# Kernel tuning notes

Hardware: AMD Instinct MI355X
Metric: run time of the kernel (lower is better)

Reference implementation:

```python
import jax, jax.numpy as jnp
import numpy as np

B, S, N_USERS, N_ITEMS, E = 32, 512, 10000, 10000, 128


def setup_inputs() -> dict:
    key = jax.random.key(0)
    ks = jax.random.split(key, 8)
    users = jax.random.randint(ks[0], (B, S), 0, N_USERS, dtype=jnp.int32)
    items = jax.random.randint(ks[1], (B, S), 0, N_ITEMS, dtype=jnp.int32)
    user_mem0 = jax.random.normal(ks[2], (B, N_USERS, E), dtype=jnp.float32)
    item_mem0 = jax.random.normal(ks[3], (B, N_ITEMS, E), dtype=jnp.float32)
    # GRUCell(2E, E): w_ih (3E, 2E), w_hh (3E, E)
    w_ih = jax.random.normal(ks[4], (3 * E, 2 * E), dtype=jnp.float32) * 0.05
    w_hh = jax.random.normal(ks[5], (3 * E, E), dtype=jnp.float32) * 0.05
    b_ih = jax.random.normal(ks[6], (3 * E,), dtype=jnp.float32) * 0.05
    b_hh = jax.random.normal(ks[7], (3 * E,), dtype=jnp.float32) * 0.05
    return {"users": users, "items": items, "user_mem0": user_mem0,
            "item_mem0": item_mem0, "w_ih": w_ih, "w_hh": w_hh,
            "b_ih": b_ih, "b_hh": b_hh}


def _gru_cell(x, h, w_ih, w_hh, b_ih, b_hh):
    # torch.nn.GRUCell semantics
    gi = x @ w_ih.T + b_ih  # (B, 3E)
    gh = h @ w_hh.T + b_hh  # (B, 3E)
    i_r, i_z, i_n = jnp.split(gi, 3, axis=-1)
    h_r, h_z, h_n = jnp.split(gh, 3, axis=-1)
    r = jax.nn.sigmoid(i_r + h_r)
    z = jax.nn.sigmoid(i_z + h_z)
    n = jnp.tanh(i_n + r * h_n)
    return (1.0 - z) * n + z * h


def reference(users, items, user_mem0, item_mem0, w_ih, w_hh, b_ih, b_hh):
    batch = jnp.arange(users.shape[0])

    def step(carry, uv):
        um, im = carry
        u, it = uv  # (B,), (B,)
        ue = um[batch, u]   # gather (B, E)
        ie = im[batch, it]  # gather (B, E)
        xu = jnp.concatenate([ue, ie], axis=-1)
        xi = jnp.concatenate([ie, ue], axis=-1)
        nu = _gru_cell(xu, ue, w_ih, w_hh, b_ih, b_hh)
        ni = _gru_cell(xi, ie, w_ih, w_hh, b_ih, b_hh)
        um = um.at[batch, u].set(nu)   # scatter write
        im = im.at[batch, it].set(ni)  # scatter write
        return (um, im), (nu, ni)

    (_, _), (u_out, i_out) = jax.lax.scan(
        step, (user_mem0, item_mem0), (users.T, items.T))
    # (S, B, E) -> (B, S, E)
    return jnp.transpose(u_out, (1, 0, 2)), jnp.transpose(i_out, (1, 0, 2))
```

## Files before the change

### kernel.cpp

```cpp
#include <hip/hip_runtime.h>

#define NB 32
#define NS 512
#define NE 128
#define NU 10000

#define WS_PREVU 0
#define WS_PREVI 16384
#define WS_RCNT  32768
#define WS_LCNT  32864
#define WS_GL    32896
#define WS_LATE  82048
#define WS_WBF   98432

typedef __attribute__((ext_vector_type(8))) short bf16x8;
typedef __attribute__((ext_vector_type(4))) float f32x4;

__device__ __forceinline__ unsigned short f2bf(float f) {
    unsigned int u = __float_as_uint(f);
    u += 0x7fff + ((u >> 16) & 1);
    return (unsigned short)(u >> 16);
}

#define BARRIER() do { \
    asm volatile("s_waitcnt lgkmcnt(0)" ::: "memory"); \
    __builtin_amdgcn_s_barrier(); \
    __builtin_amdgcn_sched_barrier(0); \
} while (0)

__global__ __launch_bounds__(512) void prep_kernel(
    const int* __restrict__ users, const int* __restrict__ items,
    const float* __restrict__ w_ih, const float* __restrict__ w_hh, int* ws)
{
    const int blk = blockIdx.x, tid = threadIdx.x;
    if (blk >= 32) {
        const int base = (blk - 32) * 4096 + tid * 8;
        const int r = base >> 7, k = base & 127;
        const float* src;
        if (r < 384)      src = w_ih + (size_t)r * 256 + k;
        else if (r < 768) src = w_ih + (size_t)(r - 384) * 256 + 128 + k;
        else              src = w_hh + (size_t)(r - 768) * 128 + k;
        unsigned short* wbf = (unsigned short*)(ws + WS_WBF);
#pragma unroll
        for (int j = 0; j < 8; ++j) wbf[base + j] = f2bf(src[j]);
        return;
    }
    const int b = blk;
    __shared__ int s_u[NS], s_i[NS];
    __shared__ unsigned char s_r[NS];
    __shared__ int cnt[3], s_chg;
    s_u[tid] = users[b * NS + tid];
    s_i[tid] = items[b * NS + tid];
    if (tid < 3) cnt[tid] = 0;
    __syncthreads();
    const int mu = s_u[tid], mi = s_i[tid];
    int pu = -1, pi = -1;
    for (int u = tid - 1; u >= 0 && pu < 0; u -= 8) {
        int vals[8];
#pragma unroll
        for (int j = 0; j < 8; ++j) {
            const int uu = u - j;
            vals[j] = (uu >= 0) ? s_u[uu] : -1;
        }
#pragma unroll
        for (int j = 0; j < 8; ++j)
            if (pu < 0 && vals[j] == mu) pu = u - j;
    }
    for (int u = tid - 1; u >= 0 && pi < 0; u -= 8) {
        int vals[8];
#pragma unroll
        for (int j = 0; j < 8; ++j) {
            const int uu = u - j;
            vals[j] = (uu >= 0) ? s_i[uu] : -1;
        }
#pragma unroll
        for (int j = 0; j < 8; ++j)
            if (pi < 0 && vals[j] == mi) pi = u - j;
    }
    ws[WS_PREVU + (b << 9) + tid] = pu;
    ws[WS_PREVI + (b << 9) + tid] = pi;
    s_r[tid] = (pu < 0 && pi < 0) ? 0 : 255;
    __syncthreads();
    for (int pass = 0; pass < 16; ++pass) {
        if (tid == 0) s_chg = 0;
        __syncthreads();
        if (s_r[tid] == 255) {
            const int ru = pu < 0 ? -1 : (int)s_r[pu];
            const int ri = pi < 0 ? -1 : (int)s_r[pi];
            if (ru != 255 && ri != 255) {
                int rr = 1 + (ru > ri ? ru : ri);
                if (rr > 3) rr = 3;
                s_r[tid] = (unsigned char)rr;
                s_chg = 1;
            }
        }
        __syncthreads();
        if (!s_chg) break;
    }
    const int r = s_r[tid];
    if (r < 3) {
        const int slot = atomicAdd(&cnt[r], 1);
        ws[WS_GL + (r * 32 + b) * 512 + slot] = tid;
    }
    __syncthreads();
    if (tid < 3) ws[WS_RCNT + tid * 32 + b] = cnt[tid];
    if (tid == 0) {
        int n = 0;
        for (int t = 0; t < NS; ++t)
            if (s_r[t] >= 3) { ws[WS_LATE + (b << 9) + n] = t; ++n; }
        ws[WS_LCNT + b] = n;
    }
}

__global__ __launch_bounds__(512, 1) void round_gemm(
    const int* __restrict__ users, const int* __restrict__ items,
    const float* __restrict__ umem0, const float* __restrict__ imem0,
    const float* __restrict__ b_ih, const float* __restrict__ b_hh,
    const int* __restrict__ ws, float* uout, float* iout, int r)
{
    const int b = blockIdx.x & 31, sblk = blockIdx.x >> 5;
    const int cnt = ws[WS_RCNT + r * 32 + b];
    const int nch = (cnt + 7) >> 3;
    if (sblk >= nch) return;
    const int tid = threadIdx.x;
    const int lane = tid & 63, wave = tid >> 6;
    const int col = lane & 15, kgrp = lane >> 4;

    __shared__ __align__(16) float yl[16 * 1156];
    __shared__ __align__(16) float xf[16 * 132];
    __shared__ __align__(16) unsigned short xb[16 * 136];
    __shared__ float b6[768];
    __shared__ unsigned long long srcs[8][16];
    __shared__ unsigned long long hdst[8][16];

    for (int i = tid; i < 768; i += 512)
        b6[i] = i < 384 ? b_ih[i] : b_hh[i - 384];

    const unsigned short* wbf = (const unsigned short*)(ws + WS_WBF);
    bf16x8 wfrag[9][4];
#pragma unroll
    for (int m9 = 0; m9 < 9; ++m9) {
        const int row = wave * 144 + m9 * 16 + col;
#pragma unroll
        for (int kt = 0; kt < 4; ++kt)
            wfrag[m9][kt] = *(const bf16x8*)&wbf[row * 128 + kt * 32 + kgrp * 8];
    }

    const int* glist = ws + WS_GL + (r * 32 + b) * 512;
    const int* prevU = ws + WS_PREVU + (b << 9);
    const int* prevI = ws + WS_PREVI + (b << 9);

    if (tid < 128) {
        const int k = tid >> 4, idx = tid & 15;
        const int lc = sblk + k * 8;
        unsigned long long sp = 0, hd = 0;
        if (lc < nch) {
            const int j = lc * 8 + (idx >> 1);
            if (j < cnt) {
                const int t = glist[j];
                const int node = (b << 9) + t;
                const int cell = idx & 1;
                const int p = cell ? prevI[t] : prevU[t];
                const float* s;
                if (p < 0) {
                    const int ix = cell ? items[node] : users[node];
                    s = (cell ? imem0 : umem0) + ((size_t)b * NU + ix) * NE;
                } else {
                    s = (cell ? iout : uout) + ((size_t)((b << 9) + p)) * NE;
                }
                sp = (unsigned long long)s;
                hd = (unsigned long long)((cell ? iout : uout) + (size_t)node * NE);
            }
        }
        srcs[k][idx] = sp; hdst[k][idx] = hd;
    }
    BARRIER();

    const int gc = tid >> 5, ge4 = (tid & 31) * 4;
    float4 v[8];
#pragma unroll
    for (int k = 0; k < 8; ++k) {
        const float* s = (const float*)srcs[k][gc];
        v[k] = (float4){0.f, 0.f, 0.f, 0.f};
        if (s) v[k] = *(const float4*)(s + ge4);
    }

#pragma unroll
    for (int k = 0; k < 8; ++k) {
        const int lc = sblk + k * 8;
        if (lc >= nch) break;
        if (srcs[k][gc]) {
            *(float4*)&xf[gc * 132 + ge4] = v[k];
            ushort4 w4;
            w4.x = f2bf(v[k].x); w4.y = f2bf(v[k].y);
            w4.z = f2bf(v[k].z); w4.w = f2bf(v[k].w);
            *(ushort4*)&xb[gc * 136 + ge4] = w4;
        }
        BARRIER();
        {
            bf16x8 bfrag[4];
#pragma unroll
            for (int kt = 0; kt < 4; ++kt)
                bfrag[kt] = *(const bf16x8*)&xb[col * 136 + kt * 32 + kgrp * 8];
            f32x4 acc[9];
#pragma unroll
            for (int m9 = 0; m9 < 9; ++m9) acc[m9] = (f32x4){0.f, 0.f, 0.f, 0.f};
#pragma unroll
            for (int kt = 0; kt < 4; ++kt)
#pragma unroll
                for (int m9 = 0; m9 < 9; ++m9)
                    acc[m9] = __builtin_amdgcn_mfma_f32_16x16x32_bf16(
                        wfrag[m9][kt], bfrag[kt], acc[m9], 0, 0, 0);
#pragma unroll
            for (int m9 = 0; m9 < 9; ++m9)
                *(f32x4*)&yl[col * 1156 + wave * 144 + m9 * 16 + kgrp * 4] = acc[m9];
        }
        BARRIER();
#pragma unroll
        for (int it = 0; it < 4; ++it) {
            const int idx = tid + it * 512;
            const int c = idx >> 7, e = idx & 127;
            float* hb = (float*)hdst[k][c];
            if (hb) {
                const float* ys = &yl[c * 1156];
                const float* yo = &yl[(c ^ 1) * 1156];
                const float gir = ys[e]        + yo[384 + e] + b6[e];
                const float giz = ys[128 + e]  + yo[512 + e] + b6[128 + e];
                const float gin = ys[256 + e]  + yo[640 + e] + b6[256 + e];
                const float ghr = ys[768 + e]  + b6[384 + e];
                const float ghz = ys[896 + e]  + b6[512 + e];
                const float ghn = ys[1024 + e] + b6[640 + e];
                const float rr = 1.f / (1.f + __expf(-(gir + ghr)));
                const float z  = 1.f / (1.f + __expf(-(giz + ghz)));
                const float pre = gin + rr * ghn;
                const float n = 2.f / (1.f + __expf(-2.f * pre)) - 1.f;
                hb[e] = (1.f - z) * n + z * xf[c * 132 + e];
            }
        }
        BARRIER();
    }
}

__global__ __launch_bounds__(512, 1) void cleanup_kernel(
    const int* __restrict__ users, const int* __restrict__ items,
    const float* __restrict__ umem0, const float* __restrict__ imem0,
    const float* __restrict__ b_ih, const float* __restrict__ b_hh,
    const int* __restrict__ ws, float* uout, float* iout)
{
    const int b = blockIdx.x;
    const int n = ws[WS_LCNT + b];
    if (n == 0) return;
    const int tid = threadIdx.x;
    const int lane = tid & 63, wave = tid >> 6;
    const int col = lane & 15, kgrp = lane >> 4;

    __shared__ __align__(16) float yl[2][1156];
    __shared__ __align__(16) float xf[2][132];
    __shared__ __align__(16) unsigned short xb[2][136];
    __shared__ float b6[768];
    __shared__ const float* srcs[2];

    for (int i = tid; i < 768; i += 512)
        b6[i] = i < 384 ? b_ih[i] : b_hh[i - 384];

    const unsigned short* wbf = (const unsigned short*)(ws + WS_WBF);
    bf16x8 wfrag[9][4];
#pragma unroll
    for (int m9 = 0; m9 < 9; ++m9) {
        const int row = wave * 144 + m9 * 16 + col;
#pragma unroll
        for (int kt = 0; kt < 4; ++kt)
            wfrag[m9][kt] = *(const bf16x8*)&wbf[row * 128 + kt * 32 + kgrp * 8];
    }

    const int* prevU = ws + WS_PREVU + (b << 9);
    const int* prevI = ws + WS_PREVI + (b << 9);

    for (int k = 0; k < n; ++k) {
        const int t = ws[WS_LATE + (b << 9) + k];
        const int node = (b << 9) + t;
        if (tid < 2) {
            const int cell = tid;
            const int p = cell ? prevI[t] : prevU[t];
            const float* sp;
            if (p < 0) {
                const int ix = cell ? items[node] : users[node];
                sp = (cell ? imem0 : umem0) + ((size_t)b * NU + ix) * NE;
            } else {
                sp = (cell ? iout : uout) + ((size_t)((b << 9) + p)) * NE;
            }
            srcs[cell] = sp;
        }
        __syncthreads();
        if (tid < 64) {
            const int c = tid >> 5, e4 = (tid & 31) * 4;
            const float4 vv = *(const float4*)(srcs[c] + e4);
            *(float4*)&xf[c][e4] = vv;
            ushort4 w4;
            w4.x = f2bf(vv.x); w4.y = f2bf(vv.y);
            w4.z = f2bf(vv.z); w4.w = f2bf(vv.w);
            *(ushort4*)&xb[c][e4] = w4;
        }
        __syncthreads();
        {
            const int bc = col & 1;
            bf16x8 bfrag[4];
#pragma unroll
            for (int kt = 0; kt < 4; ++kt)
                bfrag[kt] = *(const bf16x8*)&xb[bc][kt * 32 + kgrp * 8];
            f32x4 acc[9];
#pragma unroll
            for (int m9 = 0; m9 < 9; ++m9) acc[m9] = (f32x4){0.f, 0.f, 0.f, 0.f};
#pragma unroll
            for (int kt = 0; kt < 4; ++kt)
#pragma unroll
                for (int m9 = 0; m9 < 9; ++m9)
                    acc[m9] = __builtin_amdgcn_mfma_f32_16x16x32_bf16(
                        wfrag[m9][kt], bfrag[kt], acc[m9], 0, 0, 0);
            if (col < 2) {
#pragma unroll
                for (int m9 = 0; m9 < 9; ++m9)
                    *(f32x4*)&yl[col][wave * 144 + m9 * 16 + kgrp * 4] = acc[m9];
            }
        }
        __syncthreads();
        if (tid < 256) {
            const int c = tid >> 7, e = tid & 127;
            const float* ys = yl[c];
            const float* yo = yl[c ^ 1];
            const float gir = ys[e]        + yo[384 + e] + b6[e];
            const float giz = ys[128 + e]  + yo[512 + e] + b6[128 + e];
            const float gin = ys[256 + e]  + yo[640 + e] + b6[256 + e];
            const float ghr = ys[768 + e]  + b6[384 + e];
            const float ghz = ys[896 + e]  + b6[512 + e];
            const float ghn = ys[1024 + e] + b6[640 + e];
            const float rr = 1.f / (1.f + __expf(-(gir + ghr)));
            const float z  = 1.f / (1.f + __expf(-(giz + ghz)));
            const float pre = gin + rr * ghn;
            const float nn = 2.f / (1.f + __expf(-2.f * pre)) - 1.f;
            (c ? iout : uout)[(size_t)node * NE + e] =
                (1.f - z) * nn + z * xf[c][e];
        }
        __threadfence();
        __syncthreads();
    }
}

extern "C" void kernel_launch(void* const* d_in, const int* in_sizes, int n_in,
                              void* d_out, int out_size, void* d_ws, size_t ws_size,
                              hipStream_t stream) {
    const int*   users = (const int*)d_in[0];
    const int*   items = (const int*)d_in[1];
    const float* umem0 = (const float*)d_in[2];
    const float* imem0 = (const float*)d_in[3];
    const float* w_ih  = (const float*)d_in[4];
    const float* w_hh  = (const float*)d_in[5];
    const float* b_ih  = (const float*)d_in[6];
    const float* b_hh  = (const float*)d_in[7];

    float* uout = (float*)d_out;
    float* iout = uout + (size_t)NB * NS * NE;
    int* ws = (int*)d_ws;

    prep_kernel<<<68, 512, 0, stream>>>(users, items, w_ih, w_hh, ws);
    round_gemm<<<256, 512, 0, stream>>>(users, items, umem0, imem0,
                                        b_ih, b_hh, ws, uout, iout, 0);
    round_gemm<<<256, 512, 0, stream>>>(users, items, umem0, imem0,
                                        b_ih, b_hh, ws, uout, iout, 1);
    round_gemm<<<256, 512, 0, stream>>>(users, items, umem0, imem0,
                                        b_ih, b_hh, ws, uout, iout, 2);
    cleanup_kernel<<<NB, 512, 0, stream>>>(users, items, umem0, imem0,
                                           b_ih, b_hh, ws, uout, iout);
}
```

Measured before the change: 135.4 us.

## Fuse round and cleanup kernels into one persistent kernel with per-node ready flags

Replaces the three per-round GEMM launches and the serial cleanup launch with a single persistent kernel. Its 256 blocks walk a flattened work list of round chunks followed by late nodes. Dependencies between steps are enforced by per-node completion flags in workspace, using spin-waits with sleep and release via atomicExch after a threadfence. This removes launch gaps and lets the late tail run on many blocks instead of one block per batch. The cost is that each chunk is now processed alone rather than eight chunks sharing one load phase, plus spin-wait overhead and a deadlock risk if the dependency order is violated.

```diff
diff --git a/kernel.cpp b/kernel.cpp
--- a/kernel.cpp
+++ b/kernel.cpp
@@ -12,6 +12,7 @@
 #define WS_GL    32896
 #define WS_LATE  82048
 #define WS_WBF   98432
+#define WS_FLAG  172160
 
 typedef __attribute__((ext_vector_type(8))) short bf16x8;
 typedef __attribute__((ext_vector_type(4))) float f32x4;
@@ -43,6 +44,8 @@
         unsigned short* wbf = (unsigned short*)(ws + WS_WBF);
 #pragma unroll
         for (int j = 0; j < 8; ++j) wbf[base + j] = f2bf(src[j]);
+        const int fidx = (blk - 32) * 512 + tid;
+        if (fidx < 16384) ws[WS_FLAG + fidx] = 0;
         return;
     }
     const int b = blk;
@@ -112,16 +115,12 @@
     }
 }
 
-__global__ __launch_bounds__(512, 1) void round_gemm(
+__global__ __launch_bounds__(512, 1) void solve_kernel(
     const int* __restrict__ users, const int* __restrict__ items,
     const float* __restrict__ umem0, const float* __restrict__ imem0,
     const float* __restrict__ b_ih, const float* __restrict__ b_hh,
-    const int* __restrict__ ws, float* uout, float* iout, int r)
+    int* ws, float* uout, float* iout)
 {
-    const int b = blockIdx.x & 31, sblk = blockIdx.x >> 5;
-    const int cnt = ws[WS_RCNT + r * 32 + b];
-    const int nch = (cnt + 7) >> 3;
-    if (sblk >= nch) return;
     const int tid = threadIdx.x;
     const int lane = tid & 63, wave = tid >> 6;
     const int col = lane & 15, kgrp = lane >> 4;
@@ -130,11 +129,13 @@
     __shared__ __align__(16) float xf[16 * 132];
     __shared__ __align__(16) unsigned short xb[16 * 136];
     __shared__ float b6[768];
-    __shared__ unsigned long long srcs[8][16];
-    __shared__ unsigned long long hdst[8][16];
+    __shared__ int s_cnt[128];
+    __shared__ unsigned long long srcs[16];
+    __shared__ unsigned long long hdst[16];
 
     for (int i = tid; i < 768; i += 512)
         b6[i] = i < 384 ? b_ih[i] : b_hh[i - 384];
+    if (tid < 128) s_cnt[tid] = ws[WS_RCNT + tid];
 
     const unsigned short* wbf = (const unsigned short*)(ws + WS_WBF);
     bf16x8 wfrag[9][4];
@@ -145,58 +146,71 @@
         for (int kt = 0; kt < 4; ++kt)
             wfrag[m9][kt] = *(const bf16x8*)&wbf[row * 128 + kt * 32 + kgrp * 8];
     }
-
-    const int* glist = ws + WS_GL + (r * 32 + b) * 512;
-    const int* prevU = ws + WS_PREVU + (b << 9);
-    const int* prevI = ws + WS_PREVI + (b << 9);
-
-    if (tid < 128) {
-        const int k = tid >> 4, idx = tid & 15;
-        const int lc = sblk + k * 8;
-        unsigned long long sp = 0, hd = 0;
-        if (lc < nch) {
-            const int j = lc * 8 + (idx >> 1);
-            if (j < cnt) {
-                const int t = glist[j];
+    __syncthreads();
+
+    for (int v = blockIdx.x; v < 22528; v += 256) {
+        int base, n, b;
+        if (v < 6144) {
+            const int r = v >> 11, lc = v & 63;
+            b = (v >> 6) & 31;
+            const int cnt = s_cnt[r * 32 + b];
+            const int nch = (cnt + 7) >> 3;
+            if (lc >= nch) continue;
+            base = WS_GL + (r * 32 + b) * 512 + lc * 8;
+            n = cnt - lc * 8; if (n > 8) n = 8;
+        } else {
+            const int v2 = v - 6144, k = v2 & 511;
+            b = v2 >> 9;
+            if (k >= s_cnt[96 + b]) continue;
+            base = WS_LATE + (b << 9) + k;
+            n = 1;
+        }
+
+        int haspar = 0;
+        if (tid < 16) {
+            const int j = tid >> 1;
+            unsigned long long sp = 0, hd = 0;
+            if (j < n) {
+                const int t = ws[base + j];
                 const int node = (b << 9) + t;
-                const int cell = idx & 1;
-                const int p = cell ? prevI[t] : prevU[t];
+                const int cell = tid & 1;
+                const int p = ws[(cell ? WS_PREVI : WS_PREVU) + (b << 9) + t];
                 const float* s;
                 if (p < 0) {
                     const int ix = cell ? items[node] : users[node];
                     s = (cell ? imem0 : umem0) + ((size_t)b * NU + ix) * NE;
                 } else {
                     s = (cell ? iout : uout) + ((size_t)((b << 9) + p)) * NE;
+                    haspar = 1;
+                    int* fp = ws + WS_FLAG + (b << 9) + p;
+                    int spins = 0;
+                    while (atomicAdd(fp, 0) == 0) {
+                        __builtin_amdgcn_s_sleep(2);
+                        if (++spins > (1 << 24)) break;
+                    }
                 }
                 sp = (unsigned long long)s;
                 hd = (unsigned long long)((cell ? iout : uout) + (size_t)node * NE);
             }
-        }
-        srcs[k][idx] = sp; hdst[k][idx] = hd;
-    }
-    BARRIER();
-
-    const int gc = tid >> 5, ge4 = (tid & 31) * 4;
-    float4 v[8];
-#pragma unroll
-    for (int k = 0; k < 8; ++k) {
-        const float* s = (const float*)srcs[k][gc];
-        v[k] = (float4){0.f, 0.f, 0.f, 0.f};
-        if (s) v[k] = *(const float4*)(s + ge4);
-    }
-
-#pragma unroll
-    for (int k = 0; k < 8; ++k) {
-        const int lc = sblk + k * 8;
-        if (lc >= nch) break;
-        if (srcs[k][gc]) {
-            *(float4*)&xf[gc * 132 + ge4] = v[k];
-            ushort4 w4;
-            w4.x = f2bf(v[k].x); w4.y = f2bf(v[k].y);
-            w4.z = f2bf(v[k].z); w4.w = f2bf(v[k].w);
-            *(ushort4*)&xb[gc * 136 + ge4] = w4;
+            srcs[tid] = sp; hdst[tid] = hd;
+        }
+        if (__syncthreads_count(haspar))
+            __threadfence();
+
+        {
+            const int c = tid >> 5, e4 = (tid & 31) * 4;
+            const float* s = (const float*)srcs[c];
+            if (s) {
+                const float4 vv = *(const float4*)(s + e4);
+                *(float4*)&xf[c * 132 + e4] = vv;
+                ushort4 w4;
+                w4.x = f2bf(vv.x); w4.y = f2bf(vv.y);
+                w4.z = f2bf(vv.z); w4.w = f2bf(vv.w);
+                *(ushort4*)&xb[c * 136 + e4] = w4;
+            }
         }
         BARRIER();
+
         {
             bf16x8 bfrag[4];
 #pragma unroll
@@ -216,11 +230,12 @@
                 *(f32x4*)&yl[col * 1156 + wave * 144 + m9 * 16 + kgrp * 4] = acc[m9];
         }
         BARRIER();
+
 #pragma unroll
         for (int it = 0; it < 4; ++it) {
             const int idx = tid + it * 512;
             const int c = idx >> 7, e = idx & 127;
-            float* hb = (float*)hdst[k][c];
+            float* hb = (float*)hdst[c];
             if (hb) {
                 const float* ys = &yl[c * 1156];
                 const float* yo = &yl[(c ^ 1) * 1156];
@@ -233,116 +248,17 @@
                 const float rr = 1.f / (1.f + __expf(-(gir + ghr)));
                 const float z  = 1.f / (1.f + __expf(-(giz + ghz)));
                 const float pre = gin + rr * ghn;
-                const float n = 2.f / (1.f + __expf(-2.f * pre)) - 1.f;
-                hb[e] = (1.f - z) * n + z * xf[c * 132 + e];
-            }
-        }
-        BARRIER();
-    }
-}
-
-__global__ __launch_bounds__(512, 1) void cleanup_kernel(
-    const int* __restrict__ users, const int* __restrict__ items,
-    const float* __restrict__ umem0, const float* __restrict__ imem0,
-    const float* __restrict__ b_ih, const float* __restrict__ b_hh,
-    const int* __restrict__ ws, float* uout, float* iout)
-{
-    const int b = blockIdx.x;
-    const int n = ws[WS_LCNT + b];
-    if (n == 0) return;
-    const int tid = threadIdx.x;
-    const int lane = tid & 63, wave = tid >> 6;
-    const int col = lane & 15, kgrp = lane >> 4;
-
-    __shared__ __align__(16) float yl[2][1156];
-    __shared__ __align__(16) float xf[2][132];
-    __shared__ __align__(16) unsigned short xb[2][136];
-    __shared__ float b6[768];
-    __shared__ const float* srcs[2];
-
-    for (int i = tid; i < 768; i += 512)
-        b6[i] = i < 384 ? b_ih[i] : b_hh[i - 384];
-
-    const unsigned short* wbf = (const unsigned short*)(ws + WS_WBF);
-    bf16x8 wfrag[9][4];
-#pragma unroll
-    for (int m9 = 0; m9 < 9; ++m9) {
-        const int row = wave * 144 + m9 * 16 + col;
-#pragma unroll
-        for (int kt = 0; kt < 4; ++kt)
-            wfrag[m9][kt] = *(const bf16x8*)&wbf[row * 128 + kt * 32 + kgrp * 8];
-    }
-
-    const int* prevU = ws + WS_PREVU + (b << 9);
-    const int* prevI = ws + WS_PREVI + (b << 9);
-
-    for (int k = 0; k < n; ++k) {
-        const int t = ws[WS_LATE + (b << 9) + k];
-        const int node = (b << 9) + t;
-        if (tid < 2) {
-            const int cell = tid;
-            const int p = cell ? prevI[t] : prevU[t];
-            const float* sp;
-            if (p < 0) {
-                const int ix = cell ? items[node] : users[node];
-                sp = (cell ? imem0 : umem0) + ((size_t)b * NU + ix) * NE;
-            } else {
-                sp = (cell ? iout : uout) + ((size_t)((b << 9) + p)) * NE;
-            }
-            srcs[cell] = sp;
-        }
-        __syncthreads();
-        if (tid < 64) {
-            const int c = tid >> 5, e4 = (tid & 31) * 4;
-            const float4 vv = *(const float4*)(srcs[c] + e4);
-            *(float4*)&xf[c][e4] = vv;
-            ushort4 w4;
-            w4.x = f2bf(vv.x); w4.y = f2bf(vv.y);
-            w4.z = f2bf(vv.z); w4.w = f2bf(vv.w);
-            *(ushort4*)&xb[c][e4] = w4;
-        }
-        __syncthreads();
-        {
-            const int bc = col & 1;
-            bf16x8 bfrag[4];
-#pragma unroll
-            for (int kt = 0; kt < 4; ++kt)
-                bfrag[kt] = *(const bf16x8*)&xb[bc][kt * 32 + kgrp * 8];
-            f32x4 acc[9];
-#pragma unroll
-            for (int m9 = 0; m9 < 9; ++m9) acc[m9] = (f32x4){0.f, 0.f, 0.f, 0.f};
-#pragma unroll
-            for (int kt = 0; kt < 4; ++kt)
-#pragma unroll
-                for (int m9 = 0; m9 < 9; ++m9)
-                    acc[m9] = __builtin_amdgcn_mfma_f32_16x16x32_bf16(
-                        wfrag[m9][kt], bfrag[kt], acc[m9], 0, 0, 0);
-            if (col < 2) {
-#pragma unroll
-                for (int m9 = 0; m9 < 9; ++m9)
-                    *(f32x4*)&yl[col][wave * 144 + m9 * 16 + kgrp * 4] = acc[m9];
-            }
-        }
-        __syncthreads();
-        if (tid < 256) {
-            const int c = tid >> 7, e = tid & 127;
-            const float* ys = yl[c];
-            const float* yo = yl[c ^ 1];
-            const float gir = ys[e]        + yo[384 + e] + b6[e];
-            const float giz = ys[128 + e]  + yo[512 + e] + b6[128 + e];
-            const float gin = ys[256 + e]  + yo[640 + e] + b6[256 + e];
-            const float ghr = ys[768 + e]  + b6[384 + e];
-            const float ghz = ys[896 + e]  + b6[512 + e];
-            const float ghn = ys[1024 + e] + b6[640 + e];
-            const float rr = 1.f / (1.f + __expf(-(gir + ghr)));
-            const float z  = 1.f / (1.f + __expf(-(giz + ghz)));
-            const float pre = gin + rr * ghn;
-            const float nn = 2.f / (1.f + __expf(-2.f * pre)) - 1.f;
-            (c ? iout : uout)[(size_t)node * NE + e] =
-                (1.f - z) * nn + z * xf[c][e];
-        }
+                const float nn = 2.f / (1.f + __expf(-2.f * pre)) - 1.f;
+                hb[e] = (1.f - z) * nn + z * xf[c * 132 + e];
+            }
+        }
+
         __threadfence();
         __syncthreads();
+        if (tid < n) {
+            const int t = ws[base + tid];
+            atomicExch(ws + WS_FLAG + (b << 9) + t, 1);
+        }
     }
 }
 
@@ -363,12 +279,6 @@
     int* ws = (int*)d_ws;
 
     prep_kernel<<<68, 512, 0, stream>>>(users, items, w_ih, w_hh, ws);
-    round_gemm<<<256, 512, 0, stream>>>(users, items, umem0, imem0,
-                                        b_ih, b_hh, ws, uout, iout, 0);
-    round_gemm<<<256, 512, 0, stream>>>(users, items, umem0, imem0,
-                                        b_ih, b_hh, ws, uout, iout, 1);
-    round_gemm<<<256, 512, 0, stream>>>(users, items, umem0, imem0,
-                                        b_ih, b_hh, ws, uout, iout, 2);
-    cleanup_kernel<<<NB, 512, 0, stream>>>(users, items, umem0, imem0,
-                                           b_ih, b_hh, ws, uout, iout);
-}
+    solve_kernel<<<256, 512, 0, stream>>>(users, items, umem0, imem0,
+                                          b_ih, b_hh, ws, uout, iout);
+}
```

Measured after the change: 525.8 us. +288.3%, slower.

## Merge rounds 1-2 and cleanup into one per-batch finish kernel

Applied to the files above, without the earlier changes.

Keeps a wide round-0 kernel and replaces the round-1, round-2 and cleanup launches with a single per-batch kernel. That kernel walks rounds 1 and 2 in chunks of 8 steps, then the late steps one at a time. The intent is to save two kernel launches and their grid-wide drains. The cost is that rounds 1 and 2 now run on only 32 blocks instead of up to 256. The round-0 kernel also drops register prefetching of all chunks in favour of a simple per-chunk loop with plain __syncthreads.

```diff
diff --git a/kernel.cpp b/kernel.cpp
--- a/kernel.cpp
+++ b/kernel.cpp
@@ -21,12 +21,6 @@
     u += 0x7fff + ((u >> 16) & 1);
     return (unsigned short)(u >> 16);
 }
-
-#define BARRIER() do { \
-    asm volatile("s_waitcnt lgkmcnt(0)" ::: "memory"); \
-    __builtin_amdgcn_s_barrier(); \
-    __builtin_amdgcn_sched_barrier(0); \
-} while (0)
 
 __global__ __launch_bounds__(512) void prep_kernel(
     const int* __restrict__ users, const int* __restrict__ items,
@@ -112,14 +106,14 @@
     }
 }
 
-__global__ __launch_bounds__(512, 1) void round_gemm(
+__global__ __launch_bounds__(512, 1) void rg0_kernel(
     const int* __restrict__ users, const int* __restrict__ items,
     const float* __restrict__ umem0, const float* __restrict__ imem0,
     const float* __restrict__ b_ih, const float* __restrict__ b_hh,
-    const int* __restrict__ ws, float* uout, float* iout, int r)
+    const int* __restrict__ ws, float* uout, float* iout)
 {
     const int b = blockIdx.x & 31, sblk = blockIdx.x >> 5;
-    const int cnt = ws[WS_RCNT + r * 32 + b];
+    const int cnt = ws[WS_RCNT + b];
     const int nch = (cnt + 7) >> 3;
     if (sblk >= nch) return;
     const int tid = threadIdx.x;
@@ -130,8 +124,8 @@
     __shared__ __align__(16) float xf[16 * 132];
     __shared__ __align__(16) unsigned short xb[16 * 136];
     __shared__ float b6[768];
-    __shared__ unsigned long long srcs[8][16];
-    __shared__ unsigned long long hdst[8][16];
+    __shared__ unsigned long long srcs[16];
+    __shared__ unsigned long long hdst[16];
 
     for (int i = tid; i < 768; i += 512)
         b6[i] = i < 384 ? b_ih[i] : b_hh[i - 384];
@@ -146,57 +140,37 @@
             wfrag[m9][kt] = *(const bf16x8*)&wbf[row * 128 + kt * 32 + kgrp * 8];
     }
 
-    const int* glist = ws + WS_GL + (r * 32 + b) * 512;
-    const int* prevU = ws + WS_PREVU + (b << 9);
-    const int* prevI = ws + WS_PREVI + (b << 9);
-
-    if (tid < 128) {
-        const int k = tid >> 4, idx = tid & 15;
-        const int lc = sblk + k * 8;
-        unsigned long long sp = 0, hd = 0;
-        if (lc < nch) {
-            const int j = lc * 8 + (idx >> 1);
+    const int* glist = ws + WS_GL + b * 512;
+
+    for (int lc = sblk; lc < nch; lc += 8) {
+        if (tid < 16) {
+            const int j = lc * 8 + (tid >> 1);
+            unsigned long long sp = 0, hd = 0;
             if (j < cnt) {
                 const int t = glist[j];
                 const int node = (b << 9) + t;
-                const int cell = idx & 1;
-                const int p = cell ? prevI[t] : prevU[t];
-                const float* s;
-                if (p < 0) {
-                    const int ix = cell ? items[node] : users[node];
-                    s = (cell ? imem0 : umem0) + ((size_t)b * NU + ix) * NE;
-                } else {
-                    s = (cell ? iout : uout) + ((size_t)((b << 9) + p)) * NE;
-                }
-                sp = (unsigned long long)s;
+                const int cell = tid & 1;
+                const int ix = cell ? items[node] : users[node];
+                sp = (unsigned long long)((cell ? imem0 : umem0)
+                                          + ((size_t)b * NU + ix) * NE);
                 hd = (unsigned long long)((cell ? iout : uout) + (size_t)node * NE);
             }
-        }
-        srcs[k][idx] = sp; hdst[k][idx] = hd;
-    }
-    BARRIER();
-
-    const int gc = tid >> 5, ge4 = (tid & 31) * 4;
-    float4 v[8];
-#pragma unroll
-    for (int k = 0; k < 8; ++k) {
-        const float* s = (const float*)srcs[k][gc];
-        v[k] = (float4){0.f, 0.f, 0.f, 0.f};
-        if (s) v[k] = *(const float4*)(s + ge4);
-    }
-
-#pragma unroll
-    for (int k = 0; k < 8; ++k) {
-        const int lc = sblk + k * 8;
-        if (lc >= nch) break;
-        if (srcs[k][gc]) {
-            *(float4*)&xf[gc * 132 + ge4] = v[k];
-            ushort4 w4;
-            w4.x = f2bf(v[k].x); w4.y = f2bf(v[k].y);
-            w4.z = f2bf(v[k].z); w4.w = f2bf(v[k].w);
-            *(ushort4*)&xb[gc * 136 + ge4] = w4;
-        }
-        BARRIER();
+            srcs[tid] = sp; hdst[tid] = hd;
+        }
+        __syncthreads();
+        {
+            const int c = tid >> 5, e4 = (tid & 31) * 4;
+            const float* s = (const float*)srcs[c];
+            if (s) {
+                const float4 vv = *(const float4*)(s + e4);
+                *(float4*)&xf[c * 132 + e4] = vv;
+                ushort4 w4;
+                w4.x = f2bf(vv.x); w4.y = f2bf(vv.y);
+                w4.z = f2bf(vv.z); w4.w = f2bf(vv.w);
+                *(ushort4*)&xb[c * 136 + e4] = w4;
+            }
+        }
+        __syncthreads();
         {
             bf16x8 bfrag[4];
 #pragma unroll
@@ -215,12 +189,12 @@
             for (int m9 = 0; m9 < 9; ++m9)
                 *(f32x4*)&yl[col * 1156 + wave * 144 + m9 * 16 + kgrp * 4] = acc[m9];
         }
-        BARRIER();
+        __syncthreads();
 #pragma unroll
         for (int it = 0; it < 4; ++it) {
             const int idx = tid + it * 512;
             const int c = idx >> 7, e = idx & 127;
-            float* hb = (float*)hdst[k][c];
+            float* hb = (float*)hdst[c];
             if (hb) {
                 const float* ys = &yl[c * 1156];
                 const float* yo = &yl[(c ^ 1) * 1156];
@@ -233,32 +207,36 @@
                 const float rr = 1.f / (1.f + __expf(-(gir + ghr)));
                 const float z  = 1.f / (1.f + __expf(-(giz + ghz)));
                 const float pre = gin + rr * ghn;
-                const float n = 2.f / (1.f + __expf(-2.f * pre)) - 1.f;
-                hb[e] = (1.f - z) * n + z * xf[c * 132 + e];
-            }
-        }
-        BARRIER();
-    }
-}
-
-__global__ __launch_bounds__(512, 1) void cleanup_kernel(
+                const float nn = 2.f / (1.f + __expf(-2.f * pre)) - 1.f;
+                hb[e] = (1.f - z) * nn + z * xf[c * 132 + e];
+            }
+        }
+        __syncthreads();
+    }
+}
+
+__global__ __launch_bounds__(512, 1) void finish_kernel(
     const int* __restrict__ users, const int* __restrict__ items,
     const float* __restrict__ umem0, const float* __restrict__ imem0,
     const float* __restrict__ b_ih, const float* __restrict__ b_hh,
     const int* __restrict__ ws, float* uout, float* iout)
 {
     const int b = blockIdx.x;
-    const int n = ws[WS_LCNT + b];
-    if (n == 0) return;
     const int tid = threadIdx.x;
     const int lane = tid & 63, wave = tid >> 6;
     const int col = lane & 15, kgrp = lane >> 4;
 
-    __shared__ __align__(16) float yl[2][1156];
-    __shared__ __align__(16) float xf[2][132];
-    __shared__ __align__(16) unsigned short xb[2][136];
+    const int cnt1 = ws[WS_RCNT + 32 + b];
+    const int cnt2 = ws[WS_RCNT + 64 + b];
+    const int cntL = ws[WS_LCNT + b];
+    if (cnt1 + cnt2 + cntL == 0) return;
+
+    __shared__ __align__(16) float yl[16 * 1156];
+    __shared__ __align__(16) float xf[16 * 132];
+    __shared__ __align__(16) unsigned short xb[16 * 136];
     __shared__ float b6[768];
-    __shared__ const float* srcs[2];
+    __shared__ unsigned long long srcs[16];
+    __shared__ unsigned long long hdst[16];
 
     for (int i = tid; i < 768; i += 512)
         b6[i] = i < 384 ? b_ih[i] : b_hh[i - 384];
@@ -276,73 +254,90 @@
     const int* prevU = ws + WS_PREVU + (b << 9);
     const int* prevI = ws + WS_PREVI + (b << 9);
 
-    for (int k = 0; k < n; ++k) {
-        const int t = ws[WS_LATE + (b << 9) + k];
-        const int node = (b << 9) + t;
-        if (tid < 2) {
-            const int cell = tid;
-            const int p = cell ? prevI[t] : prevU[t];
-            const float* sp;
-            if (p < 0) {
-                const int ix = cell ? items[node] : users[node];
-                sp = (cell ? imem0 : umem0) + ((size_t)b * NU + ix) * NE;
-            } else {
-                sp = (cell ? iout : uout) + ((size_t)((b << 9) + p)) * NE;
-            }
-            srcs[cell] = sp;
-        }
-        __syncthreads();
-        if (tid < 64) {
-            const int c = tid >> 5, e4 = (tid & 31) * 4;
-            const float4 vv = *(const float4*)(srcs[c] + e4);
-            *(float4*)&xf[c][e4] = vv;
-            ushort4 w4;
-            w4.x = f2bf(vv.x); w4.y = f2bf(vv.y);
-            w4.z = f2bf(vv.z); w4.w = f2bf(vv.w);
-            *(ushort4*)&xb[c][e4] = w4;
-        }
-        __syncthreads();
-        {
-            const int bc = col & 1;
-            bf16x8 bfrag[4];
-#pragma unroll
-            for (int kt = 0; kt < 4; ++kt)
-                bfrag[kt] = *(const bf16x8*)&xb[bc][kt * 32 + kgrp * 8];
-            f32x4 acc[9];
-#pragma unroll
-            for (int m9 = 0; m9 < 9; ++m9) acc[m9] = (f32x4){0.f, 0.f, 0.f, 0.f};
-#pragma unroll
-            for (int kt = 0; kt < 4; ++kt)
+    for (int ph = 0; ph < 3; ++ph) {
+        int base, cntn, step;
+        if (ph == 0)      { cntn = cnt1; base = WS_GL + (32 + b) * 512;  step = 8; }
+        else if (ph == 1) { cntn = cnt2; base = WS_GL + (64 + b) * 512;  step = 8; }
+        else              { cntn = cntL; base = WS_LATE + (b << 9);      step = 1; }
+        for (int j0 = 0; j0 < cntn; j0 += step) {
+            const int n = (cntn - j0 < step) ? (cntn - j0) : step;
+            if (tid < 16) {
+                const int jj = tid >> 1;
+                unsigned long long sp = 0, hd = 0;
+                if (jj < n) {
+                    const int t = ws[base + j0 + jj];
+                    const int node = (b << 9) + t;
+                    const int cell = tid & 1;
+                    const int p = cell ? prevI[t] : prevU[t];
+                    const float* s;
+                    if (p < 0) {
+                        const int ix = cell ? items[node] : users[node];
+                        s = (cell ? imem0 : umem0) + ((size_t)b * NU + ix) * NE;
+                    } else {
+                        s = (cell ? iout : uout) + ((size_t)((b << 9) + p)) * NE;
+                    }
+                    sp = (unsigned long long)s;
+                    hd = (unsigned long long)((cell ? iout : uout) + (size_t)node * NE);
+                }
+                srcs[tid] = sp; hdst[tid] = hd;
+            }
+            __syncthreads();
+            {
+                const int c = tid >> 5, e4 = (tid & 31) * 4;
+                const float* s = (const float*)srcs[c];
+                if (s) {
+                    const float4 vv = *(const float4*)(s + e4);
+                    *(float4*)&xf[c * 132 + e4] = vv;
+                    ushort4 w4;
+                    w4.x = f2bf(vv.x); w4.y = f2bf(vv.y);
+                    w4.z = f2bf(vv.z); w4.w = f2bf(vv.w);
+                    *(ushort4*)&xb[c * 136 + e4] = w4;
+                }
+            }
+            __syncthreads();
+            {
+                bf16x8 bfrag[4];
+#pragma unroll
+                for (int kt = 0; kt < 4; ++kt)
+                    bfrag[kt] = *(const bf16x8*)&xb[col * 136 + kt * 32 + kgrp * 8];
+                f32x4 acc[9];
+#pragma unroll
+                for (int m9 = 0; m9 < 9; ++m9) acc[m9] = (f32x4){0.f, 0.f, 0.f, 0.f};
+#pragma unroll
+                for (int kt = 0; kt < 4; ++kt)
+#pragma unroll
+                    for (int m9 = 0; m9 < 9; ++m9)
+                        acc[m9] = __builtin_amdgcn_mfma_f32_16x16x32_bf16(
+                            wfrag[m9][kt], bfrag[kt], acc[m9], 0, 0, 0);
 #pragma unroll
                 for (int m9 = 0; m9 < 9; ++m9)
-                    acc[m9] = __builtin_amdgcn_mfma_f32_16x16x32_bf16(
-                        wfrag[m9][kt], bfrag[kt], acc[m9], 0, 0, 0);
-            if (col < 2) {
-#pragma unroll
-                for (int m9 = 0; m9 < 9; ++m9)
-                    *(f32x4*)&yl[col][wave * 144 + m9 * 16 + kgrp * 4] = acc[m9];
-            }
-        }
-        __syncthreads();
-        if (tid < 256) {
-            const int c = tid >> 7, e = tid & 127;
-            const float* ys = yl[c];
-            const float* yo = yl[c ^ 1];
-            const float gir = ys[e]        + yo[384 + e] + b6[e];
-            const float giz = ys[128 + e]  + yo[512 + e] + b6[128 + e];
-            const float gin = ys[256 + e]  + yo[640 + e] + b6[256 + e];
-            const float ghr = ys[768 + e]  + b6[384 + e];
-            const float ghz = ys[896 + e]  + b6[512 + e];
-            const float ghn = ys[1024 + e] + b6[640 + e];
-            const float rr = 1.f / (1.f + __expf(-(gir + ghr)));
-            const float z  = 1.f / (1.f + __expf(-(giz + ghz)));
-            const float pre = gin + rr * ghn;
-            const float nn = 2.f / (1.f + __expf(-2.f * pre)) - 1.f;
-            (c ? iout : uout)[(size_t)node * NE + e] =
-                (1.f - z) * nn + z * xf[c][e];
-        }
-        __threadfence();
-        __syncthreads();
+                    *(f32x4*)&yl[col * 1156 + wave * 144 + m9 * 16 + kgrp * 4] = acc[m9];
+            }
+            __syncthreads();
+#pragma unroll
+            for (int it = 0; it < 4; ++it) {
+                const int idx = tid + it * 512;
+                const int c = idx >> 7, e = idx & 127;
+                float* hb = (float*)hdst[c];
+                if (hb) {
+                    const float* ys = &yl[c * 1156];
+                    const float* yo = &yl[(c ^ 1) * 1156];
+                    const float gir = ys[e]        + yo[384 + e] + b6[e];
+                    const float giz = ys[128 + e]  + yo[512 + e] + b6[128 + e];
+                    const float gin = ys[256 + e]  + yo[640 + e] + b6[256 + e];
+                    const float ghr = ys[768 + e]  + b6[384 + e];
+                    const float ghz = ys[896 + e]  + b6[512 + e];
+                    const float ghn = ys[1024 + e] + b6[640 + e];
+                    const float rr = 1.f / (1.f + __expf(-(gir + ghr)));
+                    const float z  = 1.f / (1.f + __expf(-(giz + ghz)));
+                    const float pre = gin + rr * ghn;
+                    const float nn = 2.f / (1.f + __expf(-2.f * pre)) - 1.f;
+                    hb[e] = (1.f - z) * nn + z * xf[c * 132 + e];
+                }
+            }
+            __threadfence();
+            __syncthreads();
+        }
     }
 }
 
@@ -363,12 +358,8 @@
     int* ws = (int*)d_ws;
 
     prep_kernel<<<68, 512, 0, stream>>>(users, items, w_ih, w_hh, ws);
-    round_gemm<<<256, 512, 0, stream>>>(users, items, umem0, imem0,
-                                        b_ih, b_hh, ws, uout, iout, 0);
-    round_gemm<<<256, 512, 0, stream>>>(users, items, umem0, imem0,
-                                        b_ih, b_hh, ws, uout, iout, 1);
-    round_gemm<<<256, 512, 0, stream>>>(users, items, umem0, imem0,
-                                        b_ih, b_hh, ws, uout, iout, 2);
-    cleanup_kernel<<<NB, 512, 0, stream>>>(users, items, umem0, imem0,
-                                           b_ih, b_hh, ws, uout, iout);
-}
+    rg0_kernel<<<256, 512, 0, stream>>>(users, items, umem0, imem0,
+                                        b_ih, b_hh, ws, uout, iout);
+    finish_kernel<<<NB, 512, 0, stream>>>(users, items, umem0, imem0,
+                                          b_ih, b_hh, ws, uout, iout);
+}
```

Result: slower. 148.0 us (+9.3%).
